# Kernel tuning notes

Measured on AMD Instinct MI355X. Metric: run time of the kernel, lower is better.

The kernel has to match this reference:

```python
import jax, jax.numpy as jnp
import numpy as np
import math

DIM = 256
B, S = 4, 2048


def setup_inputs() -> dict:
    key = jax.random.key(0)
    ks = jax.random.split(key, 8)
    h = DIM // 2
    return {
        "features": jax.random.normal(ks[0], (B, S, DIM), dtype=jnp.float32),
        "W1": jax.random.normal(ks[1], (DIM, h), dtype=jnp.float32) / np.sqrt(DIM),
        "b1": jnp.zeros((h,), dtype=jnp.float32),
        "ln_g": jnp.ones((h,), dtype=jnp.float32),
        "ln_b": jnp.zeros((h,), dtype=jnp.float32),
        "W2": jax.random.normal(ks[2], (h, 1), dtype=jnp.float32) / np.sqrt(h),
        "b2": jnp.zeros((1,), dtype=jnp.float32),
        "target_entropy": jnp.full((1,), math.log(DIM), dtype=jnp.float32),
        "temperature": jnp.ones((1,), dtype=jnp.float32),
    }


def _compute_entropy(features, temperature):
    b, s, d = features.shape
    x = features.reshape(-1, d)  # [N, D]
    sq = jnp.sum(x * x, axis=-1)  # [N]
    # squared euclidean distance (cdist(...)**2), clamped for numerical safety
    d2 = jnp.maximum(sq[:, None] + sq[None, :] - 2.0 * (x @ x.T), 0.0)  # [N, N]
    kernel = jnp.exp(-d2 / (2.0 * temperature[0] ** 2))
    probs = kernel / jnp.sum(kernel, axis=-1, keepdims=True)
    entropy = -jnp.sum(probs * jnp.log(probs + 1e-6), axis=-1)
    return entropy.reshape(b, s)


def _entropy_estimator(features, W1, b1, ln_g, ln_b, W2, b2):
    h = features @ W1 + b1  # [B, S, D/2]
    mu = jnp.mean(h, axis=-1, keepdims=True)
    var = jnp.mean((h - mu) ** 2, axis=-1, keepdims=True)
    hn = (h - mu) / jnp.sqrt(var + 1e-5) * ln_g + ln_b
    hg = jax.nn.gelu(hn, approximate=False)
    return (hg @ W2 + b2).squeeze(-1)  # [B, S]


def reference(features, W1, b1, ln_g, ln_b, W2, b2, target_entropy, temperature):
    current_entropy = _compute_entropy(features, temperature)  # [B, S]
    # estimated_entropy is computed in the original forward but unused in outputs
    _est = _entropy_estimator(features, W1, b1, ln_g, ln_b, W2, b2)
    entropy_diff = current_entropy - target_entropy[0]
    control_signal = jax.nn.sigmoid(-entropy_diff / temperature[0])  # [B, S]
    controlled_features = features * control_signal[..., None]
    return controlled_features, control_signal
```

## Files before the change

### kernel.cpp

```cpp
#include <hip/hip_runtime.h>

#define N 8192
#define D 256

typedef short short8 __attribute__((ext_vector_type(8)));
typedef float f32x4 __attribute__((ext_vector_type(4)));

__device__ __forceinline__ unsigned short f2bf(float f) {
    unsigned int u = __float_as_uint(f);
    u += 0x7fffu + ((u >> 16) & 1u);
    return (unsigned short)(u >> 16);
}
__device__ __forceinline__ float bf2f(unsigned short h) {
    return __uint_as_float(((unsigned int)h) << 16);
}

__global__ __launch_bounds__(64) void k_cvt(const float* __restrict__ x,
                                            unsigned short* __restrict__ xb2,
                                            float* __restrict__ sq,
                                            float* __restrict__ Sarr,
                                            float* __restrict__ Larr) {
    const int lane = threadIdx.x & 63;
    const int c = lane & 15, q8 = lane >> 4;
    const int grp = blockIdx.x;
    const int row = grp * 16 + c;

    float ssum = 0.0f;
#pragma unroll
    for (int kk = 0; kk < 8; ++kk) {
        const float4* gp = (const float4*)(x + (size_t)row * D + kk * 32 + q8 * 8);
        float4 v0 = gp[0], v1 = gp[1];
        unsigned short h[8];
        h[0] = f2bf(v0.x); h[1] = f2bf(v0.y); h[2] = f2bf(v0.z); h[3] = f2bf(v0.w);
        h[4] = f2bf(v1.x); h[5] = f2bf(v1.y); h[6] = f2bf(v1.z); h[7] = f2bf(v1.w);
        short8 p;
#pragma unroll
        for (int i = 0; i < 8; ++i) {
            float f = bf2f(h[i]);
            ssum = fmaf(f, f, ssum);
            p[i] = (short)h[i];
        }
        ((short8*)xb2)[(grp * 8 + kk) * 64 + lane] = p;
    }
    ssum += __shfl_xor(ssum, 16, 64);
    ssum += __shfl_xor(ssum, 32, 64);
    if (q8 == 0) {
        sq[row] = ssum;
        Sarr[row] = 0.0f;
        Larr[row] = 0.0f;
    }
}

__device__ __forceinline__ void ld_b(const short8* __restrict__ xb8, int grp,
                                     int lane, short8 (&bv)[8]) {
#pragma unroll
    for (int kk = 0; kk < 8; ++kk)
        bv[kk] = xb8[(size_t)grp * 512 + kk * 64 + lane];
}

__device__ __forceinline__ void ct_compute(const short8 (&av)[4][8],
                                           const short8 (&bv)[8],
                                           float bc, const float (&ar)[16],
                                           float armax, float c2,
                                           float (&Sr)[16], float (&Mr)[16]) {
    f32x4 acc[4];
#pragma unroll
    for (int tr = 0; tr < 4; ++tr)
#pragma unroll
        for (int r = 0; r < 4; ++r) acc[tr][r] = 0.0f;

#pragma unroll
    for (int kk = 0; kk < 8; ++kk)
#pragma unroll
        for (int tr = 0; tr < 4; ++tr)
            acc[tr] = __builtin_amdgcn_mfma_f32_16x16x32_bf16(
                av[tr][kk], bv[kk], acc[tr], 0, 0, 0);

    float gmax = acc[0][0];
#pragma unroll
    for (int tr = 0; tr < 4; ++tr)
#pragma unroll
        for (int r = 0; r < 4; ++r) gmax = fmaxf(gmax, acc[tr][r]);
    const float bound = fmaf(gmax, c2, armax + bc);

    if (__any(bound >= -115.0f)) {
#pragma unroll
        for (int tr = 0; tr < 4; ++tr)
#pragma unroll
            for (int r = 0; r < 4; ++r) {
                float g = acc[tr][r];
                float t2 = fminf(fmaf(g, c2, ar[tr * 4 + r] + bc), 0.0f);
                float e = __builtin_amdgcn_exp2f(t2);
                Sr[tr * 4 + r] += e;
                Mr[tr * 4 + r] = fmaf(e, t2, Mr[tr * 4 + r]);
            }
    }
}

__global__ __launch_bounds__(256, 2) void k_gram(const unsigned short* __restrict__ xb2,
                                                 const float* __restrict__ sq,
                                                 const float* __restrict__ temp,
                                                 float* __restrict__ Sarr,
                                                 float* __restrict__ Larr) {
    const int tid = threadIdx.x;
    const int wv = tid >> 6, lane = tid & 63;
    const int q8 = lane >> 4, c = lane & 15;
    const int rowbase = blockIdx.x * 256;
    const int ybase = blockIdx.y * 256;
    const float T = temp[0];
    const float LOG2E = 1.44269504f;
    const float s2 = -LOG2E / (2.0f * T * T);
    const float c2 = -2.0f * s2;

    short8 av[4][8];
#pragma unroll
    for (int tr = 0; tr < 4; ++tr) {
        const int grp = (rowbase >> 4) + wv * 4 + tr;
#pragma unroll
        for (int kk = 0; kk < 8; ++kk)
            av[tr][kk] = ((const short8*)xb2)[(grp * 8 + kk) * 64 + lane];
    }
    float ar[16];
#pragma unroll
    for (int tr = 0; tr < 4; ++tr)
#pragma unroll
        for (int r = 0; r < 4; ++r)
            ar[tr * 4 + r] = sq[rowbase + wv * 64 + tr * 16 + q8 * 4 + r] * s2;
    float armax = ar[0];
#pragma unroll
    for (int k = 1; k < 16; ++k) armax = fmaxf(armax, ar[k]);

    float Sr[16], Mr[16];
#pragma unroll
    for (int k = 0; k < 16; ++k) { Sr[k] = 0.f; Mr[k] = 0.f; }

    const short8* xb8 = (const short8*)xb2;
    const int gbase = ybase >> 4;

    short8 bvA[8], bvB[8];
    float bcA, bcB;
    ld_b(xb8, gbase, lane, bvA);
    bcA = sq[ybase + c] * s2;

    for (int ct = 0; ct < 16; ct += 2) {
        ld_b(xb8, gbase + ct + 1, lane, bvB);
        bcB = sq[ybase + (ct + 1) * 16 + c] * s2;

        ct_compute(av, bvA, bcA, ar, armax, c2, Sr, Mr);

        const int nx = (ct + 2 < 16) ? ct + 2 : 0;
        ld_b(xb8, gbase + nx, lane, bvA);
        bcA = sq[ybase + nx * 16 + c] * s2;

        ct_compute(av, bvB, bcB, ar, armax, c2, Sr, Mr);
    }

#pragma unroll
    for (int m = 1; m <= 8; m <<= 1)
#pragma unroll
        for (int k = 0; k < 16; ++k) {
            Sr[k] += __shfl_xor(Sr[k], m, 64);
            Mr[k] += __shfl_xor(Mr[k], m, 64);
        }
    if (c == 0) {
        const float LN2 = 0.69314718f;
#pragma unroll
        for (int k = 0; k < 16; ++k) {
            int row = rowbase + wv * 64 + (k >> 2) * 16 + q8 * 4 + (k & 3);
            atomicAdd(&Sarr[row], Sr[k]);
            atomicAdd(&Larr[row], Mr[k] * LN2);
        }
    }
}

__global__ __launch_bounds__(256) void k_finish(const float* __restrict__ x,
                                                const float* __restrict__ Sarr,
                                                const float* __restrict__ Larr,
                                                const float* __restrict__ target,
                                                const float* __restrict__ temp,
                                                float* __restrict__ out) {
    const int gid = blockIdx.x * 256 + threadIdx.x;
    const int row = gid >> 6;
    float S = Sarr[row], L = Larr[row];
    float H = __logf(S) - L / S;
    float z = (H - target[0]) / temp[0];
    float cs = 1.0f / (1.0f + __expf(z));
    float4 v = ((const float4*)x)[gid];
    float4 o;
    o.x = v.x * cs; o.y = v.y * cs; o.z = v.z * cs; o.w = v.w * cs;
    ((float4*)out)[gid] = o;
    if ((gid & 63) == 0) out[(size_t)N * D + row] = cs;
}

extern "C" void kernel_launch(void* const* d_in, const int* in_sizes, int n_in,
                              void* d_out, int out_size, void* d_ws, size_t ws_size,
                              hipStream_t stream) {
    const float* x = (const float*)d_in[0];
    const float* target = (const float*)d_in[7];
    const float* temp = (const float*)d_in[8];
    float* out = (float*)d_out;

    float* wsf = (float*)d_ws;
    float* sq = wsf;
    float* Sarr = wsf + N;
    float* Larr = wsf + 2 * N;

    const size_t need = 3 * (size_t)N * sizeof(float) + (size_t)N * D * sizeof(unsigned short);
    unsigned short* xb2 = (ws_size >= need) ? (unsigned short*)(wsf + 3 * N)
                                            : (unsigned short*)d_out;

    k_cvt<<<N / 16, 64, 0, stream>>>(x, xb2, sq, Sarr, Larr);
    k_gram<<<dim3(32, 32), 256, 0, stream>>>(xb2, sq, temp, Sarr, Larr);
    k_finish<<<(N * (D / 4)) / 256, 256, 0, stream>>>(x, Sarr, Larr, target, temp, out);
}
```

Before: 113.0 us.

## Exploit Gram-matrix symmetry so each off-diagonal tile is computed once

The kernel now uses the symmetry of the pairwise distance matrix. Each pair of mirrored off-diagonal 256x256 blocks splits the column tiles between its two launches, so every off-diagonal entry is computed only once. Each computed tile adds its exp and entropy terms both to its rows, as before, and to its columns. The column sums are reduced across lanes with shuffles and added atomically per tile. This roughly halves the MFMA and exp work, in exchange for extra shuffles and global atomics inside the tile loop.

```diff
diff --git a/kernel.cpp b/kernel.cpp
--- a/kernel.cpp
+++ b/kernel.cpp
@@ -62,7 +62,10 @@
                                            const short8 (&bv)[8],
                                            float bc, const float (&ar)[16],
                                            float armax, float c2,
-                                           float (&Sr)[16], float (&Mr)[16]) {
+                                           float (&Sr)[16], float (&Mr)[16],
+                                           bool od, int colbase,
+                                           float* __restrict__ Sarr,
+                                           float* __restrict__ Larr) {
     f32x4 acc[4];
 #pragma unroll
     for (int tr = 0; tr < 4; ++tr)
@@ -84,6 +87,7 @@
     const float bound = fmaf(gmax, c2, armax + bc);
 
     if (__any(bound >= -115.0f)) {
+        float cS = 0.0f, cL = 0.0f;
 #pragma unroll
         for (int tr = 0; tr < 4; ++tr)
 #pragma unroll
@@ -93,7 +97,21 @@
                 float e = __builtin_amdgcn_exp2f(t2);
                 Sr[tr * 4 + r] += e;
                 Mr[tr * 4 + r] = fmaf(e, t2, Mr[tr * 4 + r]);
+                cS += e;
+                cL = fmaf(e, t2, cL);
             }
+        if (od) {
+            cS += __shfl_xor(cS, 16, 64);
+            cS += __shfl_xor(cS, 32, 64);
+            cL += __shfl_xor(cL, 16, 64);
+            cL += __shfl_xor(cL, 32, 64);
+            const int lane = threadIdx.x & 63;
+            if ((lane >> 4) == 0) {
+                const float LN2 = 0.69314718f;
+                atomicAdd(&Sarr[colbase + (lane & 15)], cS);
+                atomicAdd(&Larr[colbase + (lane & 15)], cL * LN2);
+            }
+        }
     }
 }
 
@@ -102,11 +120,23 @@
                                                  const float* __restrict__ temp,
                                                  float* __restrict__ Sarr,
                                                  float* __restrict__ Larr) {
+    int bx = (int)blockIdx.x, by = (int)blockIdx.y;
+    int ct0 = 0, ct1 = 16;
+    bool od;
+    if (bx == by) {
+        od = false;
+    } else if (bx < by) {
+        od = true; ct0 = 0; ct1 = 8;
+    } else {
+        int t = bx; bx = by; by = t;
+        od = true; ct0 = 8; ct1 = 16;
+    }
+
     const int tid = threadIdx.x;
     const int wv = tid >> 6, lane = tid & 63;
     const int q8 = lane >> 4, c = lane & 15;
-    const int rowbase = blockIdx.x * 256;
-    const int ybase = blockIdx.y * 256;
+    const int rowbase = bx * 256;
+    const int ybase = by * 256;
     const float T = temp[0];
     const float LOG2E = 1.44269504f;
     const float s2 = -LOG2E / (2.0f * T * T);
@@ -139,20 +169,22 @@
 
     short8 bvA[8], bvB[8];
     float bcA, bcB;
-    ld_b(xb8, gbase, lane, bvA);
-    bcA = sq[ybase + c] * s2;
-
-    for (int ct = 0; ct < 16; ct += 2) {
+    ld_b(xb8, gbase + ct0, lane, bvA);
+    bcA = sq[ybase + ct0 * 16 + c] * s2;
+
+    for (int ct = ct0; ct < ct1; ct += 2) {
         ld_b(xb8, gbase + ct + 1, lane, bvB);
         bcB = sq[ybase + (ct + 1) * 16 + c] * s2;
 
-        ct_compute(av, bvA, bcA, ar, armax, c2, Sr, Mr);
-
-        const int nx = (ct + 2 < 16) ? ct + 2 : 0;
+        ct_compute(av, bvA, bcA, ar, armax, c2, Sr, Mr,
+                   od, ybase + ct * 16, Sarr, Larr);
+
+        const int nx = (ct + 2 < ct1) ? ct + 2 : ct0;
         ld_b(xb8, gbase + nx, lane, bvA);
         bcA = sq[ybase + nx * 16 + c] * s2;
 
-        ct_compute(av, bvB, bcB, ar, armax, c2, Sr, Mr);
+        ct_compute(av, bvB, bcB, ar, armax, c2, Sr, Mr,
+                   od, ybase + (ct + 1) * 16, Sarr, Larr);
     }
 
 #pragma unroll
```

After: 115.4 us. 1.02x slower.
